# Kernel optimization log

Hardware: AMD Instinct MI355X
Metric: run time of the kernel (lower is better)

The kernel has to match this reference:

```python
import jax, jax.numpy as jnp
import numpy as np


def setup_inputs() -> dict:
    key = jax.random.key(0)
    k1, k2 = jax.random.split(key)
    b, d = 8192, 256
    x = jax.random.normal(k1, (b, d), dtype=jnp.float32)
    dc = jax.random.uniform(k2, (b, d), dtype=jnp.float32)
    dc_param = jnp.array([0.05], dtype=jnp.float32)
    return {"x": x, "dc": dc, "dc_param": dc_param}


def reference(x, dc, dc_param):
    # Faithful to torch: sim[i,j] = 1 / mean_k[(1-p)*(x[i,k]-x[j,k])^2
    #                                        + p*exp(1-dc[i,k])*exp(1-dc[j,k])]
    # Expanded to GEMMs to avoid the O(b^2*d) broadcast intermediate:
    #   mean_k (x_i - x_j)^2 = (|x_i|^2 + |x_j|^2 - 2 x_i.x_j) / d
    #   mean_k e_i[k] e_j[k] = (e_i . e_j) / d,  e = exp(1 - dc)
    b, d = x.shape
    p = dc_param[0]
    sq = jnp.sum(x * x, axis=1)                      # (b,)
    msd = (sq[:, None] + sq[None, :] - 2.0 * (x @ x.T)) / d  # (b,b)
    e = jnp.exp(1.0 - dc)                            # (b,d)
    mker = (e @ e.T) / d                             # (b,b)
    sim = 1.0 / ((1.0 - p) * msd + p * mker)
    eye = jnp.eye(b, dtype=x.dtype)
    return sim * (1.0 - eye) + eye
```

## Files before the change

kernel.cpp:

```cpp
#include <hip/hip_runtime.h>
#include <hip/hip_bf16.h>

typedef __attribute__((ext_vector_type(8))) __bf16 bf16x8;
typedef __attribute__((ext_vector_type(4))) float  f32x4;

constexpr int NROW = 8192;
constexpr int DDIM = 256;
constexpr int KDIM = 512;
constexpr int BM = 256, BN = 128, BK = 32;
constexpr int NT = KDIM / BK;
constexpr int ABYTES = BM * BK * 2;
constexpr int BBYTES = BN * BK * 2;
constexpr int BUFBYTES = ABYTES + BBYTES;

__device__ __forceinline__ void gload_lds16(const void* g, void* l) {
  __builtin_amdgcn_global_load_lds(
      (const __attribute__((address_space(1))) void*)g,
      (__attribute__((address_space(3))) void*)l, 16, 0, 0);
}

__global__ __launch_bounds__(256) void prep_kernel(
    const float* __restrict__ x, const float* __restrict__ dc,
    const float* __restrict__ pparm,
    __hip_bfloat16* __restrict__ P, float* __restrict__ s)
{
  const int row = blockIdx.x;
  const int t   = threadIdx.x;
  const float xv = x[(size_t)row * DDIM + t];
  const float ev = __expf(1.0f - dc[(size_t)row * DDIM + t]);
  P[(size_t)row * KDIM + t]        = __float2bfloat16(xv);
  P[(size_t)row * KDIM + DDIM + t] = __float2bfloat16(ev);

  float v = xv * xv;
  #pragma unroll
  for (int off = 32; off > 0; off >>= 1) v += __shfl_down(v, off, 64);
  __shared__ float red[4];
  const int lane = t & 63, wid = t >> 6;
  if (lane == 0) red[wid] = v;
  __syncthreads();
  if (t == 0) {
    const float p = pparm[0];
    s[row] = (1.0f - p) * (1.0f / (float)DDIM) * (red[0] + red[1] + red[2] + red[3]);
  }
}

__global__ void __launch_bounds__(512, 4) adj_gemm(
    const __hip_bfloat16* __restrict__ P, const float* __restrict__ s,
    const float* __restrict__ pparm, float* __restrict__ out)
{
  __shared__ __align__(16) char lds[2 * BUFBYTES];

  const float p  = pparm[0];
  const float cx = -2.0f * (1.0f - p) / (float)DDIM;
  const float ce = p / (float)DDIM;
  const float midscale = cx / ce;

  const int orig  = blockIdx.x;
  const int xcd   = orig & 7;
  const int local = orig >> 3;
  const int bi = xcd * 4 + (local & 3);
  const int bj = local >> 2;
  const int rowBase = bi * BM;
  const int colBase = bj * BN;

  const int tid  = threadIdx.x;
  const int lane = tid & 63;
  const int wid  = tid >> 6;
  const int wmrow = (wid >> 1) * 64;
  const int wnrow = (wid & 1) * 64;
  const int frow = lane & 15;
  const int kq   = lane >> 4;

  const int cb = (kq * 16) ^ ((frow & 3) << 4);

  const int rA0  = tid >> 2;
  const int gcol = ((tid & 3) * 16) ^ ((rA0 & 3) << 4);
  const char* Pc = (const char*)P;
  const char* gA0 = Pc + (size_t)(rowBase + rA0)       * (KDIM * 2) + gcol;
  const char* gA1 = Pc + (size_t)(rowBase + 128 + rA0) * (KDIM * 2) + gcol;
  const char* gB  = Pc + (size_t)(colBase + rA0)       * (KDIM * 2) + gcol;
  const int dA0 = tid * 16, dA1 = 8192 + tid * 16, dB = ABYTES + tid * 16;

#define STAGE(kk) do {                                   \
    char* _b = lds + ((kk) & 1) * BUFBYTES;              \
    const int _ko = (kk) * (BK * 2);                     \
    gload_lds16(gA0 + _ko, _b + dA0);                    \
    gload_lds16(gA1 + _ko, _b + dA1);                    \
    gload_lds16(gB  + _ko, _b + dB);                     \
  } while (0)

  STAGE(0);
  asm volatile("s_waitcnt vmcnt(0)" ::: "memory");
  asm volatile("s_barrier" ::: "memory");

  f32x4 acc[4][4];
  #pragma unroll
  for (int m = 0; m < 4; ++m)
    #pragma unroll
    for (int n = 0; n < 4; ++n)
      acc[m][n] = (f32x4){0.f, 0.f, 0.f, 0.f};

  #pragma unroll
  for (int t = 0; t < NT; ++t) {
    const char* buf  = lds + (t & 1) * BUFBYTES;
    const char* bufB = buf + ABYTES;

    if (t < NT - 1) STAGE(t + 1);

    bf16x8 a[4], b[4];
    #pragma unroll
    for (int i = 0; i < 4; ++i)
      a[i] = *(const bf16x8*)(buf + (wmrow + i * 16 + frow) * 64 + cb);
    #pragma unroll
    for (int j = 0; j < 4; ++j)
      b[j] = *(const bf16x8*)(bufB + (wnrow + j * 16 + frow) * 64 + cb);

    #pragma unroll
    for (int i = 0; i < 4; ++i)
      #pragma unroll
      for (int j = 0; j < 4; ++j)
        acc[i][j] = __builtin_amdgcn_mfma_f32_16x16x32_bf16(a[i], b[j], acc[i][j], 0, 0, 0);

    if (t == DDIM / BK - 1) {
      #pragma unroll
      for (int m = 0; m < 4; ++m)
        #pragma unroll
        for (int n = 0; n < 4; ++n)
          acc[m][n] *= midscale;
    }

    if (t < NT - 1) {
      asm volatile("s_waitcnt vmcnt(0)" ::: "memory");
      asm volatile("s_barrier" ::: "memory");
    }
  }

  const int rq = lane >> 4;
  #pragma unroll
  for (int n = 0; n < 4; ++n) {
    const int gcol_o = colBase + wnrow + n * 16 + frow;
    const float scol = s[gcol_o];
    #pragma unroll
    for (int m = 0; m < 4; ++m) {
      const int growb = rowBase + wmrow + m * 16 + rq * 4;
      #pragma unroll
      for (int r = 0; r < 4; ++r) {
        const int grow = growb + r;
        const float denom = s[grow] + scol + ce * acc[m][n][r];
        const float val = (grow == gcol_o) ? 1.0f : __builtin_amdgcn_rcpf(denom);
        out[(size_t)grow * NROW + gcol_o] = val;
      }
    }
  }
}

extern "C" void kernel_launch(void* const* d_in, const int* in_sizes, int n_in,
                              void* d_out, int out_size, void* d_ws, size_t ws_size,
                              hipStream_t stream) {
  const float* x  = (const float*)d_in[0];
  const float* dc = (const float*)d_in[1];
  const float* pp = (const float*)d_in[2];
  float* out = (float*)d_out;

  __hip_bfloat16* P = (__hip_bfloat16*)d_ws;
  float* s = (float*)((char*)d_ws + (size_t)NROW * KDIM * 2);

  prep_kernel<<<NROW, 256, 0, stream>>>(x, dc, pp, P, s);
  adj_gemm<<<(NROW / BM) * (NROW / BN), 512, 0, stream>>>(P, s, pp, out);
}
```

Baseline: 115.3 us.

## Stage epilogue through LDS for coalesced 16-byte output stores; simplify block mapping

The epilogue now writes the reciprocal results into a swizzled LDS tile in two halves, then reads them back as float4 and writes full contiguous row segments to global memory. This replaces the scattered 4-byte stores along the MFMA layout. The LDS allocation grows to 64 KB, which may reduce occupancy, and the extra barriers add sync cost. The XCD-aware block remap is also replaced by a plain row-major mapping, which changes L2 locality across XCDs.

```diff
diff --git a/kernel.cpp b/kernel.cpp
--- a/kernel.cpp
+++ b/kernel.cpp
@@ -48,18 +48,16 @@
     const __hip_bfloat16* __restrict__ P, const float* __restrict__ s,
     const float* __restrict__ pparm, float* __restrict__ out)
 {
-  __shared__ __align__(16) char lds[2 * BUFBYTES];
+  __shared__ __align__(16) char lds[65536];
 
   const float p  = pparm[0];
   const float cx = -2.0f * (1.0f - p) / (float)DDIM;
   const float ce = p / (float)DDIM;
   const float midscale = cx / ce;
 
-  const int orig  = blockIdx.x;
-  const int xcd   = orig & 7;
-  const int local = orig >> 3;
-  const int bi = xcd * 4 + (local & 3);
-  const int bj = local >> 2;
+  const int orig = blockIdx.x;
+  const int bi = orig >> 6;
+  const int bj = orig & 63;
   const int rowBase = bi * BM;
   const int colBase = bj * BN;
 
@@ -135,21 +133,42 @@
     }
   }
 
+  float* ldsf = (float*)lds;
   const int rq = lane >> 4;
+
   #pragma unroll
-  for (int n = 0; n < 4; ++n) {
-    const int gcol_o = colBase + wnrow + n * 16 + frow;
-    const float scol = s[gcol_o];
+  for (int h = 0; h < 2; ++h) {
+    __syncthreads();
     #pragma unroll
-    for (int m = 0; m < 4; ++m) {
-      const int growb = rowBase + wmrow + m * 16 + rq * 4;
+    for (int j = 0; j < 2; ++j) {
+      const int n = 2 * h + j;
+      const int gcol_o = colBase + wnrow + n * 16 + frow;
+      const float scol = s[gcol_o];
       #pragma unroll
-      for (int r = 0; r < 4; ++r) {
-        const int grow = growb + r;
-        const float denom = s[grow] + scol + ce * acc[m][n][r];
-        const float val = (grow == gcol_o) ? 1.0f : __builtin_amdgcn_rcpf(denom);
-        out[(size_t)grow * NROW + gcol_o] = val;
+      for (int m = 0; m < 4; ++m) {
+        #pragma unroll
+        for (int r = 0; r < 4; ++r) {
+          const int R = wmrow + m * 16 + rq * 4 + r;
+          const int grow = rowBase + R;
+          const float denom = s[grow] + scol + ce * acc[m][n][r];
+          const float val = (grow == gcol_o) ? 1.0f : __builtin_amdgcn_rcpf(denom);
+          const int cc = (j * 16 + frow) ^ (((R >> 2) & 1) << 4);
+          ldsf[(wid & 1) * 8192 + R * 32 + cc] = val;
+        }
       }
+    }
+    __syncthreads();
+    #pragma unroll
+    for (int i = 0; i < 8; ++i) {
+      const int idx = i * 512 + tid;
+      const int R   = idx >> 4;
+      const int q   = idx & 15;
+      const int st  = q >> 3;
+      const int qq  = q & 7;
+      const int ccs = (qq * 4) ^ (((R >> 2) & 1) << 4);
+      const f32x4 v = *(const f32x4*)&ldsf[st * 8192 + R * 32 + ccs];
+      const int col = colBase + st * 64 + h * 32 + qq * 4;
+      *(f32x4*)&out[(size_t)(rowBase + R) * NROW + col] = v;
     }
   }
 }
```

Result: slower. 119.4 us (+3.6%).
